# Kernel tuning notes

Measured on AMD Instinct MI355X. Metric: run time of the kernel, lower is better.

## Reference

```python
import jax, jax.numpy as jnp
import numpy as np

B, S, H, DFF, E, K = 2, 2048, 1024, 2048, 8, 2


def setup_inputs() -> dict:
    key = jax.random.key(0)
    ks = jax.random.split(key, 8)
    sc_h = 1.0 / np.sqrt(H)
    sc_f = 1.0 / np.sqrt(DFF)
    x = jax.random.normal(ks[0], (B, S, H), dtype=jnp.float32)
    Wg = jax.random.uniform(ks[1], (E, H), jnp.float32, -sc_h, sc_h)  # gate (no bias)
    W1 = jax.random.uniform(ks[2], (E, DFF, H), jnp.float32, -sc_h, sc_h)  # SiGLU gate proj
    b1 = jax.random.uniform(ks[3], (E, DFF), jnp.float32, -sc_h, sc_h)
    W2 = jax.random.uniform(ks[4], (E, DFF, H), jnp.float32, -sc_h, sc_h)  # SiGLU value proj
    b2 = jax.random.uniform(ks[5], (E, DFF), jnp.float32, -sc_h, sc_h)
    W3 = jax.random.uniform(ks[6], (E, H, DFF), jnp.float32, -sc_f, sc_f)  # down proj
    b3 = jax.random.uniform(ks[7], (E, H), jnp.float32, -sc_f, sc_f)
    return {"x": x, "Wg": Wg, "W1": W1, "b1": b1, "W2": W2, "b2": b2, "W3": W3, "b3": b3}


def _moe(x, Wg, W1, b1, W2, b2, W3, b3):
    Bm, Sm, Hm = x.shape
    xt = x.reshape(-1, Hm)  # [T, H]
    gout = xt @ Wg.T  # [T, E]
    topv, topi = jax.lax.top_k(gout, K)  # [T, K]
    w = jax.nn.softmax(topv, axis=-1)  # [T, K]
    # combine weights per expert: comb[t, e] = sum_k w[t,k] * 1[topi[t,k]==e]
    comb = jnp.einsum('tke,tk->te', jax.nn.one_hot(topi, E, dtype=x.dtype), w)  # [T, E]
    # dense per-expert FFN (fixed-shape equivalent of the gather/scatter loop)
    g = jnp.einsum('th,efh->etf', xt, W1) + b1[:, None, :]  # [E, T, DFF]
    v = jnp.einsum('th,efh->etf', xt, W2) + b2[:, None, :]
    h = jax.nn.silu(g) * v  # SiGLU
    eo = jnp.einsum('etf,ehf->eth', h, W3) + b3[:, None, :]  # [E, T, H]
    out = jnp.einsum('eth,te->th', eo, comb)
    return out.reshape(Bm, Sm, Hm)


def reference(x, Wg, W1, b1, W2, b2, W3, b3):
    return _moe(x, Wg, W1, b1, W2, b2, W3, b3)
```

## Files before the change

### kernel.cpp

```cpp
#include <hip/hip_runtime.h>
#include <hip/hip_bf16.h>

#define T_TOK 4096
#define H_DIM 1024
#define DFF_D 2048
#define E_NUM 8
#define K_TOP 2
#define MAXJOBS64 136
#define MAXJOBS128 72

typedef __attribute__((ext_vector_type(8))) short s16x8;
typedef __attribute__((ext_vector_type(4))) float f32x4;

__device__ __forceinline__ ushort f2bf(float f) {
    unsigned u = __float_as_uint(f);
    u = (u + 0x7FFFu + ((u >> 16) & 1u)) >> 16;
    return (ushort)u;
}

__device__ __forceinline__ float bf2f(short s) {
    return __uint_as_float(((unsigned)(ushort)s) << 16);
}

__device__ __forceinline__ void glds16(const ushort* g, ushort* l) {
    __builtin_amdgcn_global_load_lds(
        (const __attribute__((address_space(1))) unsigned*)g,
        (__attribute__((address_space(3))) unsigned*)l, 16, 0, 0);
}

__device__ __forceinline__ s16x8 lds_frag(const ushort* base, int row, int bytecol) {
    int byte = row * 128 + (bytecol ^ ((row & 7) << 4));
    return *(const s16x8*)((const char*)base + byte);
}

__device__ __forceinline__ void cvt8(const float* p, ushort* dst, size_t i) {
    float4 a = ((const float4*)(p + i * 8))[0];
    float4 b = ((const float4*)(p + i * 8))[1];
    union { ushort us[8]; uint4 q; } o;
    o.us[0] = f2bf(a.x); o.us[1] = f2bf(a.y); o.us[2] = f2bf(a.z); o.us[3] = f2bf(a.w);
    o.us[4] = f2bf(b.x); o.us[5] = f2bf(b.y); o.us[6] = f2bf(b.z); o.us[7] = f2bf(b.w);
    ((uint4*)dst)[i] = o.q;
}

__global__ __launch_bounds__(256) void cvt_kernel(
    const float* __restrict__ in, ushort* __restrict__ out, int n8)
{
    int i = blockIdx.x * blockDim.x + threadIdx.x;
    const int stride = gridDim.x * blockDim.x;
    for (; i < n8; i += stride) cvt8(in, out, i);
}

__global__ __launch_bounds__(256) void cvt3_kernel(
    const float* __restrict__ x,  ushort* __restrict__ xbf,
    const float* __restrict__ W1, ushort* __restrict__ w1bf,
    const float* __restrict__ W2, ushort* __restrict__ w2bf)
{
    const int nW = E_NUM * DFF_D * H_DIM / 8;
    const int nX = T_TOK * H_DIM / 8;
    const int total = 2 * nW + nX;
    int i = blockIdx.x * blockDim.x + threadIdx.x;
    const int stride = gridDim.x * blockDim.x;
    for (; i < total; i += stride) {
        if (i < nW)            cvt8(W1, w1bf, i);
        else if (i < 2 * nW)   cvt8(W2, w2bf, i - nW);
        else                   cvt8(x,  xbf,  i - 2 * nW);
    }
}

__global__ __launch_bounds__(256) void gate_kernel(
    const float* __restrict__ x, const float* __restrict__ Wg,
    int* __restrict__ topi_packed, float* __restrict__ wt_slot)
{
    const int t = blockIdx.x * 4 + (threadIdx.x >> 6);
    const int lane = threadIdx.x & 63;
    const float* xr = x + (size_t)t * H_DIM;
    float xv[16];
    #pragma unroll
    for (int j = 0; j < 16; ++j) xv[j] = xr[j * 64 + lane];

    float score[E_NUM];
    #pragma unroll
    for (int e = 0; e < E_NUM; ++e) {
        const float* wr = Wg + e * H_DIM;
        float p = 0.f;
        #pragma unroll
        for (int j = 0; j < 16; ++j) p += xv[j] * wr[j * 64 + lane];
        #pragma unroll
        for (int s = 32; s >= 1; s >>= 1) p += __shfl_xor(p, s, 64);
        score[e] = p;
    }
    if (lane == 0) {
        int i0 = 0;
        #pragma unroll
        for (int e = 1; e < E_NUM; ++e) if (score[e] > score[i0]) i0 = e;
        int i1 = (i0 == 0) ? 1 : 0;
        #pragma unroll
        for (int e = 0; e < E_NUM; ++e)
            if (e != i0 && score[e] > score[i1]) i1 = e;
        float e1 = expf(score[i1] - score[i0]);
        float w0 = 1.f / (1.f + e1);
        float w1 = e1 / (1.f + e1);
        topi_packed[t] = i0 | (i1 << 8);
        wt_slot[t * K_TOP + 0] = w0;
        wt_slot[t * K_TOP + 1] = w1;
    }
}

__global__ __launch_bounds__(256) void build_lists(
    const int* __restrict__ topi_packed,
    int* __restrict__ cnt, int* __restrict__ tok_list, int* __restrict__ slot_list)
{
    const int e = blockIdx.x;
    __shared__ int lcnt;
    if (threadIdx.x == 0) lcnt = 0;
    __syncthreads();
    for (int t = threadIdx.x; t < T_TOK; t += 256) {
        int pk = topi_packed[t];
        int i0 = pk & 0xff;
        int i1 = (pk >> 8) & 0xff;
        if (i0 == e) {
            int p = atomicAdd(&lcnt, 1);
            tok_list[e * T_TOK + p] = t;
            slot_list[e * T_TOK + p] = t * K_TOP + 0;
        }
        if (i1 == e) {
            int p = atomicAdd(&lcnt, 1);
            tok_list[e * T_TOK + p] = t;
            slot_list[e * T_TOK + p] = t * K_TOP + 1;
        }
    }
    __syncthreads();
    if (threadIdx.x == 0) cnt[e] = lcnt;
}

__global__ void build_jobs(const int* __restrict__ cnt,
                           int* __restrict__ jobs64, int* __restrict__ jobs128,
                           int* __restrict__ njobs)
{
    if (threadIdx.x == 0 && blockIdx.x == 0) {
        int n = 0, n2 = 0;
        for (int e = 0; e < E_NUM; ++e) {
            int mt = (cnt[e] + 63) >> 6;
            for (int m = 0; m < mt; ++m) jobs64[n++] = (e << 16) | m;
            int mt2 = (cnt[e] + 127) >> 7;
            for (int m = 0; m < mt2; ++m) jobs128[n2++] = (e << 16) | m;
        }
        njobs[0] = n;
        njobs[1] = n2;
    }
}

__global__ __launch_bounds__(256) void up_kernel(
    const ushort* __restrict__ xbf,
    const ushort* __restrict__ w1bf, const float* __restrict__ b1,
    const ushort* __restrict__ w2bf, const float* __restrict__ b2,
    const int* __restrict__ cnt, const int* __restrict__ tok_list,
    const int* __restrict__ slot_list, const float* __restrict__ wt_slot,
    const int* __restrict__ jobs128, const int* __restrict__ njobs,
    ushort* __restrict__ h)
{
    if ((int)blockIdx.y >= njobs[1]) return;
    const int jb = jobs128[blockIdx.y];
    const int e = jb >> 16;
    const int mbase = (jb & 0xffff) * 128;
    const int M = cnt[e];
    const int nbase = blockIdx.x * 64;
    const int tid = threadIdx.x;
    const int lane = tid & 63;
    const int w = tid >> 6;

    __shared__ ushort As[128 * 64];
    __shared__ ushort B1s[64 * 64];
    __shared__ ushort B2s[64 * 64];

    const ushort* srcA[4];
    const ushort* srcB1[2];
    const ushort* srcB2[2];
    #pragma unroll
    for (int j = 0; j < 4; ++j) {
        int o = j * 4096 + tid * 16;
        int r = o >> 7;
        int cb = (o & 127) ^ ((r & 7) << 4);
        int lpos = mbase + r; if (lpos > M - 1) lpos = M - 1;
        int tok = tok_list[e * T_TOK + lpos];
        srcA[j] = xbf + (size_t)tok * H_DIM + (cb >> 1);
    }
    #pragma unroll
    for (int j = 0; j < 2; ++j) {
        int o = j * 4096 + tid * 16;
        int r = o >> 7;
        int cb = (o & 127) ^ ((r & 7) << 4);
        srcB1[j] = w1bf + ((size_t)e * DFF_D + nbase + r) * H_DIM + (cb >> 1);
        srcB2[j] = w2bf + ((size_t)e * DFF_D + nbase + r) * H_DIM + (cb >> 1);
    }

    const f32x4 zero = {0.f, 0.f, 0.f, 0.f};
    f32x4 accg[2][4], accv[2][4];
    #pragma unroll
    for (int mi = 0; mi < 2; ++mi)
        #pragma unroll
        for (int ni = 0; ni < 4; ++ni) { accg[mi][ni] = zero; accv[mi][ni] = zero; }

    const int r16 = lane & 15;
    const int g4  = lane >> 4;
    const int cb0 = g4 * 16;

    for (int k0 = 0; k0 < H_DIM; k0 += 64) {
        #pragma unroll
        for (int j = 0; j < 4; ++j)
            glds16(srcA[j] + k0, &As[j * 2048 + tid * 8]);
        #pragma unroll
        for (int j = 0; j < 2; ++j) {
            glds16(srcB1[j] + k0, &B1s[j * 2048 + tid * 8]);
            glds16(srcB2[j] + k0, &B2s[j * 2048 + tid * 8]);
        }
        __syncthreads();
        #pragma unroll
        for (int kk = 0; kk < 2; ++kk) {
            s16x8 bf1[4], bf2[4];
            #pragma unroll
            for (int ni = 0; ni < 4; ++ni) {
                bf1[ni] = lds_frag(B1s, ni * 16 + r16, kk * 64 + cb0);
                bf2[ni] = lds_frag(B2s, ni * 16 + r16, kk * 64 + cb0);
            }
            #pragma unroll
            for (int mi = 0; mi < 2; ++mi) {
                s16x8 af = lds_frag(As, w * 32 + mi * 16 + r16, kk * 64 + cb0);
                #pragma unroll
                for (int ni = 0; ni < 4; ++ni) {
                    accg[mi][ni] = __builtin_amdgcn_mfma_f32_16x16x32_bf16(af, bf1[ni], accg[mi][ni], 0, 0, 0);
                    accv[mi][ni] = __builtin_amdgcn_mfma_f32_16x16x32_bf16(af, bf2[ni], accv[mi][ni], 0, 0, 0);
                }
            }
        }
        __syncthreads();
    }

    #pragma unroll
    for (int mi = 0; mi < 2; ++mi) {
        #pragma unroll
        for (int j = 0; j < 4; ++j) {
            int p = mbase + w * 32 + mi * 16 + g4 * 4 + j;
            if (p < M) {
                int slot = slot_list[e * T_TOK + p];
                float wgt = wt_slot[slot];
                #pragma unroll
                for (int ni = 0; ni < 4; ++ni) {
                    int col = nbase + ni * 16 + r16;
                    float g = accg[mi][ni][j] + b1[e * DFF_D + col];
                    float v = accv[mi][ni][j] + b2[e * DFF_D + col];
                    float s = g / (1.f + __expf(-g));
                    h[(size_t)slot * DFF_D + col] = f2bf(wgt * s * v);
                }
            }
        }
    }
}

__global__ __launch_bounds__(128) void down_kernel(
    const ushort* __restrict__ h,
    const ushort* __restrict__ w3bf,
    const int* __restrict__ cnt, const int* __restrict__ slot_list,
    const int* __restrict__ jobs128, const int* __restrict__ njobs,
    ushort* __restrict__ eo)
{
    if ((int)blockIdx.y >= njobs[1]) return;
    const int jb = jobs128[blockIdx.y];
    const int e = jb >> 16;
    const int mbase = (jb & 0xffff) * 128;
    const int M = cnt[e];
    const int nbase = blockIdx.x * 64;
    const int tid = threadIdx.x;
    const int lane = tid & 63;
    const int w = tid >> 6;

    __shared__ ushort As[128 * 64];
    __shared__ ushort Bs[64 * 64];

    const ushort* srcA[8];
    #pragma unroll
    for (int j = 0; j < 8; ++j) {
        int o = j * 2048 + tid * 16;
        int r = o >> 7;
        int cb = (o & 127) ^ ((r & 7) << 4);
        int lpos = mbase + r; if (lpos > M - 1) lpos = M - 1;
        int slot = slot_list[e * T_TOK + lpos];
        srcA[j] = h + (size_t)slot * DFF_D + (cb >> 1);
    }
    const ushort* srcB[4];
    #pragma unroll
    for (int j = 0; j < 4; ++j) {
        int o = j * 2048 + tid * 16;
        int r = o >> 7;
        int cb = (o & 127) ^ ((r & 7) << 4);
        srcB[j] = w3bf + ((size_t)e * H_DIM + nbase + r) * DFF_D + (cb >> 1);
    }

    const f32x4 zero = {0.f, 0.f, 0.f, 0.f};
    f32x4 acc[4][4];
    #pragma unroll
    for (int mi = 0; mi < 4; ++mi)
        #pragma unroll
        for (int ni = 0; ni < 4; ++ni) acc[mi][ni] = zero;

    const int r16 = lane & 15;
    const int g4  = lane >> 4;
    const int cb0 = g4 * 16;

    for (int k0 = 0; k0 < DFF_D; k0 += 64) {
        #pragma unroll
        for (int j = 0; j < 8; ++j)
            glds16(srcA[j] + k0, &As[j * 1024 + tid * 8]);
        #pragma unroll
        for (int j = 0; j < 4; ++j)
            glds16(srcB[j] + k0, &Bs[j * 1024 + tid * 8]);
        __syncthreads();
        #pragma unroll
        for (int kk = 0; kk < 2; ++kk) {
            s16x8 bf[4];
            #pragma unroll
            for (int ni = 0; ni < 4; ++ni)
                bf[ni] = lds_frag(Bs, ni * 16 + r16, kk * 64 + cb0);
            #pragma unroll
            for (int mi = 0; mi < 4; ++mi) {
                s16x8 af = lds_frag(As, w * 64 + mi * 16 + r16, kk * 64 + cb0);
                #pragma unroll
                for (int ni = 0; ni < 4; ++ni)
                    acc[mi][ni] = __builtin_amdgcn_mfma_f32_16x16x32_bf16(af, bf[ni], acc[mi][ni], 0, 0, 0);
            }
        }
        __syncthreads();
    }

    #pragma unroll
    for (int mi = 0; mi < 4; ++mi) {
        #pragma unroll
        for (int j = 0; j < 4; ++j) {
            int p = mbase + w * 64 + mi * 16 + g4 * 4 + j;
            if (p < M) {
                int slot = slot_list[e * T_TOK + p];
                #pragma unroll
                for (int ni = 0; ni < 4; ++ni) {
                    int col = nbase + ni * 16 + r16;
                    eo[(size_t)slot * H_DIM + col] = f2bf(acc[mi][ni][j]);
                }
            }
        }
    }
}

__global__ __launch_bounds__(256) void combine_kernel(
    const ushort* __restrict__ eo, const int* __restrict__ topi_packed,
    const float* __restrict__ wt_slot, const float* __restrict__ b3,
    float* __restrict__ out)
{
    const int i = blockIdx.x * 256 + threadIdx.x;
    const int t = i >> 7;
    const int c0 = (i & 127) * 8;
    const int pk = topi_packed[t];
    const int e0 = pk & 0xff, e1 = (pk >> 8) & 0xff;
    const float w0 = wt_slot[2 * t], w1 = wt_slot[2 * t + 1];
    s16x8 a = *(const s16x8*)(eo + (size_t)(2 * t) * H_DIM + c0);
    s16x8 b = *(const s16x8*)(eo + (size_t)(2 * t + 1) * H_DIM + c0);
    const float4* p0 = (const float4*)(b3 + e0 * H_DIM + c0);
    const float4* p1 = (const float4*)(b3 + e1 * H_DIM + c0);
    float4 b0a = p0[0], b0b = p0[1];
    float4 b1a = p1[0], b1b = p1[1];
    float4 r0, r1;
    r0.x = bf2f(a[0]) + bf2f(b[0]) + w0 * b0a.x + w1 * b1a.x;
    r0.y = bf2f(a[1]) + bf2f(b[1]) + w0 * b0a.y + w1 * b1a.y;
    r0.z = bf2f(a[2]) + bf2f(b[2]) + w0 * b0a.z + w1 * b1a.z;
    r0.w = bf2f(a[3]) + bf2f(b[3]) + w0 * b0a.w + w1 * b1a.w;
    r1.x = bf2f(a[4]) + bf2f(b[4]) + w0 * b0b.x + w1 * b1b.x;
    r1.y = bf2f(a[5]) + bf2f(b[5]) + w0 * b0b.y + w1 * b1b.y;
    r1.z = bf2f(a[6]) + bf2f(b[6]) + w0 * b0b.z + w1 * b1b.z;
    r1.w = bf2f(a[7]) + bf2f(b[7]) + w0 * b0b.w + w1 * b1b.w;
    float4* op = (float4*)(out + (size_t)t * H_DIM + c0);
    op[0] = r0;
    op[1] = r1;
}

extern "C" void kernel_launch(void* const* d_in, const int* in_sizes, int n_in,
                              void* d_out, int out_size, void* d_ws, size_t ws_size,
                              hipStream_t stream) {
    const float* x  = (const float*)d_in[0];
    const float* Wg = (const float*)d_in[1];
    const float* W1 = (const float*)d_in[2];
    const float* b1 = (const float*)d_in[3];
    const float* W2 = (const float*)d_in[4];
    const float* b2 = (const float*)d_in[5];
    const float* W3 = (const float*)d_in[6];
    const float* b3 = (const float*)d_in[7];
    float* out = (float*)d_out;

    char* ws = (char*)d_ws;
    int*   cnt       = (int*)(ws);
    int*   njobs     = (int*)(ws + 64);
    int*   jobs64    = (int*)(ws + 128);
    int*   jobs128   = (int*)(ws + 704);
    int*   tok_list  = (int*)(ws + 1024);
    int*   slot_list = (int*)(ws + 1024 + E_NUM * T_TOK * 4);
    float* wt_slot   = (float*)(ws + 1024 + 2 * E_NUM * T_TOK * 4);
    int*   topi      = (int*)(ws + 320 * 1024);
    ushort* xbf  = (ushort*)(ws + (size_t)1  * (1u << 20));
    ushort* w1bf = (ushort*)(ws + (size_t)16 * (1u << 20));
    ushort* w2bf = (ushort*)(ws + (size_t)48 * (1u << 20));
    ushort* hbuf = (ushort*)(ws + (size_t)80 * (1u << 20));
    ushort* w3bf = w2bf;
    ushort* eobf = w1bf;

    cvt3_kernel<<<2048, 256, 0, stream>>>(x, xbf, W1, w1bf, W2, w2bf);

    gate_kernel<<<T_TOK / 4, 256, 0, stream>>>(x, Wg, topi, wt_slot);
    build_lists<<<E_NUM, 256, 0, stream>>>(topi, cnt, tok_list, slot_list);
    build_jobs<<<1, 64, 0, stream>>>(cnt, jobs64, jobs128, njobs);

    dim3 gup(DFF_D / 64, MAXJOBS128);
    up_kernel<<<gup, 256, 0, stream>>>(xbf, w1bf, b1, w2bf, b2, cnt, tok_list,
                                       slot_list, wt_slot, jobs128, njobs, hbuf);

    cvt_kernel<<<2048, 256, 0, stream>>>(W3, w3bf, E_NUM * H_DIM * DFF_D / 8);

    dim3 gdn(H_DIM / 64, MAXJOBS128);
    down_kernel<<<gdn, 128, 0, stream>>>(hbuf, w3bf, cnt, slot_list,
                                         jobs128, njobs, eobf);

    combine_kernel<<<T_TOK * H_DIM / 8 / 256, 256, 0, stream>>>(eobf, topi, wt_slot, b3, out);
}
```

Before: 260.3 us.

## Fuse x bf16 cast into gate, merge W3 cast, retile up-proj into 2x2 warps

The x-to-bf16 conversion moves into the gate kernel, which already reads x. When the workspace is large enough, the W3 conversion joins the W1/W2 conversion launch so the separate cvt launch between the up and down kernels goes away. The up kernel now stacks the W1 and W2 tiles into a single 128-row B tile and uses a 2x2 warp grid with 4x4 MFMA tiles, giving more reuse of each fragment. The SiLU half is passed through LDS to the warps holding the value half, which adds an extra LDS round trip and barrier in the epilogue.

```diff
diff --git a/kernel.cpp b/kernel.cpp
--- a/kernel.cpp
+++ b/kernel.cpp
@@ -50,26 +50,26 @@
     for (; i < n8; i += stride) cvt8(in, out, i);
 }
 
-__global__ __launch_bounds__(256) void cvt3_kernel(
-    const float* __restrict__ x,  ushort* __restrict__ xbf,
+__global__ __launch_bounds__(256) void cvtW_kernel(
     const float* __restrict__ W1, ushort* __restrict__ w1bf,
-    const float* __restrict__ W2, ushort* __restrict__ w2bf)
+    const float* __restrict__ W2, ushort* __restrict__ w2bf,
+    const float* __restrict__ W3, ushort* __restrict__ w3bf)
 {
     const int nW = E_NUM * DFF_D * H_DIM / 8;
-    const int nX = T_TOK * H_DIM / 8;
-    const int total = 2 * nW + nX;
+    const int total = (W3 != nullptr) ? 3 * nW : 2 * nW;
     int i = blockIdx.x * blockDim.x + threadIdx.x;
     const int stride = gridDim.x * blockDim.x;
     for (; i < total; i += stride) {
         if (i < nW)            cvt8(W1, w1bf, i);
         else if (i < 2 * nW)   cvt8(W2, w2bf, i - nW);
-        else                   cvt8(x,  xbf,  i - 2 * nW);
+        else                   cvt8(W3, w3bf, i - 2 * nW);
     }
 }
 
 __global__ __launch_bounds__(256) void gate_kernel(
     const float* __restrict__ x, const float* __restrict__ Wg,
-    int* __restrict__ topi_packed, float* __restrict__ wt_slot)
+    int* __restrict__ topi_packed, float* __restrict__ wt_slot,
+    ushort* __restrict__ xbf)
 {
     const int t = blockIdx.x * 4 + (threadIdx.x >> 6);
     const int lane = threadIdx.x & 63;
@@ -77,6 +77,10 @@
     float xv[16];
     #pragma unroll
     for (int j = 0; j < 16; ++j) xv[j] = xr[j * 64 + lane];
+
+    ushort* xo = xbf + (size_t)t * H_DIM;
+    #pragma unroll
+    for (int j = 0; j < 16; ++j) xo[j * 64 + lane] = f2bf(xv[j]);
 
     float score[E_NUM];
     #pragma unroll
@@ -168,14 +172,14 @@
     const int tid = threadIdx.x;
     const int lane = tid & 63;
     const int w = tid >> 6;
-
-    __shared__ ushort As[128 * 64];
-    __shared__ ushort B1s[64 * 64];
-    __shared__ ushort B2s[64 * 64];
+    const int wr = w >> 1, wc = w & 1;
+
+    __shared__ ushort smem[2 * 128 * 64];
+    ushort* As = smem;
+    ushort* Bs = smem + 128 * 64;
 
     const ushort* srcA[4];
-    const ushort* srcB1[2];
-    const ushort* srcB2[2];
+    const ushort* srcB[4];
     #pragma unroll
     for (int j = 0; j < 4; ++j) {
         int o = j * 4096 + tid * 16;
@@ -184,22 +188,18 @@
         int lpos = mbase + r; if (lpos > M - 1) lpos = M - 1;
         int tok = tok_list[e * T_TOK + lpos];
         srcA[j] = xbf + (size_t)tok * H_DIM + (cb >> 1);
-    }
-    #pragma unroll
-    for (int j = 0; j < 2; ++j) {
-        int o = j * 4096 + tid * 16;
-        int r = o >> 7;
-        int cb = (o & 127) ^ ((r & 7) << 4);
-        srcB1[j] = w1bf + ((size_t)e * DFF_D + nbase + r) * H_DIM + (cb >> 1);
-        srcB2[j] = w2bf + ((size_t)e * DFF_D + nbase + r) * H_DIM + (cb >> 1);
+        if (r < 64)
+            srcB[j] = w1bf + ((size_t)e * DFF_D + nbase + r) * H_DIM + (cb >> 1);
+        else
+            srcB[j] = w2bf + ((size_t)e * DFF_D + nbase + (r - 64)) * H_DIM + (cb >> 1);
     }
 
     const f32x4 zero = {0.f, 0.f, 0.f, 0.f};
-    f32x4 accg[2][4], accv[2][4];
-    #pragma unroll
-    for (int mi = 0; mi < 2; ++mi)
-        #pragma unroll
-        for (int ni = 0; ni < 4; ++ni) { accg[mi][ni] = zero; accv[mi][ni] = zero; }
+    f32x4 acc[4][4];
+    #pragma unroll
+    for (int mi = 0; mi < 4; ++mi)
+        #pragma unroll
+        for (int ni = 0; ni < 4; ++ni) acc[mi][ni] = zero;
 
     const int r16 = lane & 15;
     const int g4  = lane >> 4;
@@ -207,50 +207,67 @@
 
     for (int k0 = 0; k0 < H_DIM; k0 += 64) {
         #pragma unroll
-        for (int j = 0; j < 4; ++j)
+        for (int j = 0; j < 4; ++j) {
             glds16(srcA[j] + k0, &As[j * 2048 + tid * 8]);
-        #pragma unroll
-        for (int j = 0; j < 2; ++j) {
-            glds16(srcB1[j] + k0, &B1s[j * 2048 + tid * 8]);
-            glds16(srcB2[j] + k0, &B2s[j * 2048 + tid * 8]);
+            glds16(srcB[j] + k0, &Bs[j * 2048 + tid * 8]);
         }
         __syncthreads();
         #pragma unroll
         for (int kk = 0; kk < 2; ++kk) {
-            s16x8 bf1[4], bf2[4];
-            #pragma unroll
-            for (int ni = 0; ni < 4; ++ni) {
-                bf1[ni] = lds_frag(B1s, ni * 16 + r16, kk * 64 + cb0);
-                bf2[ni] = lds_frag(B2s, ni * 16 + r16, kk * 64 + cb0);
+            s16x8 bf[4];
+            #pragma unroll
+            for (int ni = 0; ni < 4; ++ni)
+                bf[ni] = lds_frag(Bs, wc * 64 + ni * 16 + r16, kk * 64 + cb0);
+            #pragma unroll
+            for (int mi = 0; mi < 4; ++mi) {
+                s16x8 af = lds_frag(As, wr * 64 + mi * 16 + r16, kk * 64 + cb0);
+                #pragma unroll
+                for (int ni = 0; ni < 4; ++ni)
+                    acc[mi][ni] = __builtin_amdgcn_mfma_f32_16x16x32_bf16(af, bf[ni], acc[mi][ni], 0, 0, 0);
             }
-            #pragma unroll
-            for (int mi = 0; mi < 2; ++mi) {
-                s16x8 af = lds_frag(As, w * 32 + mi * 16 + r16, kk * 64 + cb0);
-                #pragma unroll
-                for (int ni = 0; ni < 4; ++ni) {
-                    accg[mi][ni] = __builtin_amdgcn_mfma_f32_16x16x32_bf16(af, bf1[ni], accg[mi][ni], 0, 0, 0);
-                    accv[mi][ni] = __builtin_amdgcn_mfma_f32_16x16x32_bf16(af, bf2[ni], accv[mi][ni], 0, 0, 0);
-                }
-            }
         }
         __syncthreads();
     }
 
-    #pragma unroll
-    for (int mi = 0; mi < 2; ++mi) {
-        #pragma unroll
-        for (int j = 0; j < 4; ++j) {
-            int p = mbase + w * 32 + mi * 16 + g4 * 4 + j;
-            if (p < M) {
-                int slot = slot_list[e * T_TOK + p];
+    float* Ls = (float*)smem;
+    if (wc == 0) {
+        #pragma unroll
+        for (int mi = 0; mi < 4; ++mi) {
+            #pragma unroll
+            for (int j = 0; j < 4; ++j) {
+                int rl = wr * 64 + mi * 16 + g4 * 4 + j;
+                int p = mbase + rl;
+                int pc = (p < M) ? p : (M - 1);
+                int slot = slot_list[e * T_TOK + pc];
                 float wgt = wt_slot[slot];
                 #pragma unroll
                 for (int ni = 0; ni < 4; ++ni) {
                     int col = nbase + ni * 16 + r16;
-                    float g = accg[mi][ni][j] + b1[e * DFF_D + col];
-                    float v = accv[mi][ni][j] + b2[e * DFF_D + col];
-                    float s = g / (1.f + __expf(-g));
-                    h[(size_t)slot * DFF_D + col] = f2bf(wgt * s * v);
+                    float g = acc[mi][ni][j] + b1[e * DFF_D + col];
+                    float s = wgt * g / (1.f + __expf(-g));
+                    int cl = (ni * 16 + r16) ^ ((rl & 3) << 2);
+                    Ls[rl * 64 + cl] = s;
+                }
+            }
+        }
+    }
+    __syncthreads();
+    if (wc == 1) {
+        #pragma unroll
+        for (int mi = 0; mi < 4; ++mi) {
+            #pragma unroll
+            for (int j = 0; j < 4; ++j) {
+                int rl = wr * 64 + mi * 16 + g4 * 4 + j;
+                int p = mbase + rl;
+                if (p < M) {
+                    int slot = slot_list[e * T_TOK + p];
+                    #pragma unroll
+                    for (int ni = 0; ni < 4; ++ni) {
+                        int col = nbase + ni * 16 + r16;
+                        float v = acc[mi][ni][j] + b2[e * DFF_D + col];
+                        int cl = (ni * 16 + r16) ^ ((rl & 3) << 2);
+                        h[(size_t)slot * DFF_D + col] = f2bf(Ls[rl * 64 + cl] * v);
+                    }
                 }
             }
         }
@@ -406,12 +423,17 @@
     ushort* w1bf = (ushort*)(ws + (size_t)16 * (1u << 20));
     ushort* w2bf = (ushort*)(ws + (size_t)48 * (1u << 20));
     ushort* hbuf = (ushort*)(ws + (size_t)80 * (1u << 20));
-    ushort* w3bf = w2bf;
     ushort* eobf = w1bf;
 
-    cvt3_kernel<<<2048, 256, 0, stream>>>(x, xbf, W1, w1bf, W2, w2bf);
-
-    gate_kernel<<<T_TOK / 4, 256, 0, stream>>>(x, Wg, topi, wt_slot);
+    const bool bigws = ws_size >= ((size_t)145 << 20);
+    ushort* w3bf = bigws ? (ushort*)(ws + (size_t)112 * (1u << 20)) : w2bf;
+
+    if (bigws)
+        cvtW_kernel<<<2048, 256, 0, stream>>>(W1, w1bf, W2, w2bf, W3, w3bf);
+    else
+        cvtW_kernel<<<2048, 256, 0, stream>>>(W1, w1bf, W2, w2bf, nullptr, nullptr);
+
+    gate_kernel<<<T_TOK / 4, 256, 0, stream>>>(x, Wg, topi, wt_slot, xbf);
     build_lists<<<E_NUM, 256, 0, stream>>>(topi, cnt, tok_list, slot_list);
     build_jobs<<<1, 64, 0, stream>>>(cnt, jobs64, jobs128, njobs);
 
@@ -419,7 +441,8 @@
     up_kernel<<<gup, 256, 0, stream>>>(xbf, w1bf, b1, w2bf, b2, cnt, tok_list,
                                        slot_list, wt_slot, jobs128, njobs, hbuf);
 
-    cvt_kernel<<<2048, 256, 0, stream>>>(W3, w3bf, E_NUM * H_DIM * DFF_D / 8);
+    if (!bigws)
+        cvt_kernel<<<2048, 256, 0, stream>>>(W3, w3bf, E_NUM * H_DIM * DFF_D / 8);
 
     dim3 gdn(H_DIM / 64, MAXJOBS128);
     down_kernel<<<gdn, 128, 0, stream>>>(hbuf, w3bf, cnt, slot_list,
```

Result: slower. 285.7 us (+9.7%).
